# Kernel optimization log

Measured on AMD Instinct MI355X. Metric: run time of the kernel, lower is better.

The kernel has to match this reference:

```python
import jax, jax.numpy as jnp
import numpy as np

N = 40000
E = 640000
F_IN = 128
F_OUT = 128


def setup_inputs() -> dict:
    key = jax.random.key(0)
    ks = jax.random.split(key, 8)
    x = jax.random.normal(ks[0], (N, F_IN), dtype=jnp.float32)
    weight = jax.random.normal(ks[1], (F_IN, F_OUT), dtype=jnp.float32) * (1.0 / np.sqrt(F_OUT))
    node_w = jax.random.normal(ks[2], (F_IN, 1), dtype=jnp.float32)
    sem_w = jax.random.normal(ks[3], (F_IN,), dtype=jnp.float32) * (1.0 / np.sqrt(F_IN))
    bias = jax.random.normal(ks[4], (F_OUT,), dtype=jnp.float32) * 0.01
    adj_val = jax.random.uniform(ks[5], (E,), dtype=jnp.float32)
    src = jax.random.randint(ks[6], (E,), 0, N, dtype=jnp.int32)
    dst = jax.random.randint(ks[7], (E,), 0, N, dtype=jnp.int32)
    return {"x": x, "weight": weight, "node_w": node_w, "sem_w": sem_w,
            "bias": bias, "adj_val": adj_val, "src": src, "dst": dst}


def reference(x, weight, node_w, sem_w, bias, adj_val, src, dst):
    # node-level attention: per-node sigmoid scalar [N, 1]
    node_att = jax.nn.sigmoid(x @ node_w)
    # semantic-level attention: softmax over feature weight vector [F_in]
    sem_att = jax.nn.softmax(sem_w)
    # hierarchical weighting, then dense projection [N, F_out]
    support = (x * node_att * sem_att) @ weight
    # spmm(adj, support): COO aggregation, row=dst, col=src
    msg = support[src] * adj_val[:, None]  # [E, F_out]
    out = jax.ops.segment_sum(msg, dst, num_segments=N)
    return out + bias
```

## Files before the change

kernel.cpp:

```cpp
#include <hip/hip_runtime.h>
#include <hip/hip_bf16.h>

#define F 128
#define ROWS 32
#define CAP 64

typedef unsigned long long u64;

__global__ __launch_bounds__(256, 4) void support_kernel(
    const float* __restrict__ x, const float* __restrict__ weight,
    const float* __restrict__ node_w, const float* __restrict__ sem_w,
    float* __restrict__ support, int* __restrict__ cursor, int n_rows)
{
    __shared__ __align__(16) float xs[ROWS * F];
    __shared__ __align__(16) float sem[F];
    __shared__ float natt[ROWS];

    const int t = threadIdx.x;
    const int rbase = blockIdx.x * ROWS;

    if (cursor) {
        int gi = blockIdx.x * 256 + t;
        if (gi < n_rows) cursor[gi] = 0;
    }

    if (t < 64) {
        float v0 = sem_w[t], v1 = sem_w[t + 64];
        float m = fmaxf(v0, v1);
        #pragma unroll
        for (int off = 32; off; off >>= 1) m = fmaxf(m, __shfl_xor(m, off));
        float e0 = __expf(v0 - m), e1 = __expf(v1 - m);
        float ssum = e0 + e1;
        #pragma unroll
        for (int off = 32; off; off >>= 1) ssum += __shfl_xor(ssum, off);
        float inv = 1.0f / ssum;
        sem[t] = e0 * inv;
        sem[t + 64] = e1 * inv;
    }

    const int k4 = t & 31;
    float4 nw4 = ((const float4*)node_w)[k4];
    #pragma unroll
    for (int i = 0; i < 4; ++i) {
        int j = t + i * 256;
        int r = j >> 5;
        int gr = rbase + r;
        float4 v = make_float4(0.f, 0.f, 0.f, 0.f);
        if (gr < n_rows) v = ((const float4*)x)[(size_t)gr * 32 + k4];
        ((float4*)xs)[j] = v;
        float p = v.x * nw4.x + v.y * nw4.y + v.z * nw4.z + v.w * nw4.w;
        p += __shfl_xor(p, 1);  p += __shfl_xor(p, 2);  p += __shfl_xor(p, 4);
        p += __shfl_xor(p, 8);  p += __shfl_xor(p, 16);
        if ((t & 31) == 0) natt[r] = p;
    }
    __syncthreads();

    if (t < ROWS) {
        float z = natt[t];
        natt[t] = 1.0f / (1.0f + __expf(-z));
    }
    __syncthreads();

    #pragma unroll
    for (int i = 0; i < 4; ++i) {
        int j = t + i * 256;
        int r = j >> 5, kk = j & 31;
        float4 v = ((float4*)xs)[j];
        float4 s4 = ((float4*)sem)[kk];
        float a = natt[r];
        v.x *= a * s4.x; v.y *= a * s4.y; v.z *= a * s4.z; v.w *= a * s4.w;
        ((float4*)xs)[j] = v;
    }
    __syncthreads();

    const int cg = t & 31;
    const int rg = t >> 5;
    const float4* __restrict__ W4 = (const float4*)weight;
    float acc[4][4] = {};
    for (int k = 0; k < F; k += 4) {
        float4 w0 = W4[(k + 0) * 32 + cg];
        float4 w1 = W4[(k + 1) * 32 + cg];
        float4 w2 = W4[(k + 2) * 32 + cg];
        float4 w3 = W4[(k + 3) * 32 + cg];
        #pragma unroll
        for (int i = 0; i < 4; ++i) {
            float4 s = *(const float4*)&xs[(4 * rg + i) * F + k];
            acc[i][0] = fmaf(s.x, w0.x, acc[i][0]);
            acc[i][1] = fmaf(s.x, w0.y, acc[i][1]);
            acc[i][2] = fmaf(s.x, w0.z, acc[i][2]);
            acc[i][3] = fmaf(s.x, w0.w, acc[i][3]);
            acc[i][0] = fmaf(s.y, w1.x, acc[i][0]);
            acc[i][1] = fmaf(s.y, w1.y, acc[i][1]);
            acc[i][2] = fmaf(s.y, w1.z, acc[i][2]);
            acc[i][3] = fmaf(s.y, w1.w, acc[i][3]);
            acc[i][0] = fmaf(s.z, w2.x, acc[i][0]);
            acc[i][1] = fmaf(s.z, w2.y, acc[i][1]);
            acc[i][2] = fmaf(s.z, w2.z, acc[i][2]);
            acc[i][3] = fmaf(s.z, w2.w, acc[i][3]);
            acc[i][0] = fmaf(s.w, w3.x, acc[i][0]);
            acc[i][1] = fmaf(s.w, w3.y, acc[i][1]);
            acc[i][2] = fmaf(s.w, w3.z, acc[i][2]);
            acc[i][3] = fmaf(s.w, w3.w, acc[i][3]);
        }
    }

    #pragma unroll
    for (int i = 0; i < 4; ++i) {
        int r = rbase + 4 * rg + i;
        if (r < n_rows) {
            float4 o = make_float4(acc[i][0], acc[i][1], acc[i][2], acc[i][3]);
            ((float4*)support)[(size_t)r * 32 + cg] = o;
        }
    }
}

__global__ void append_kernel(const int* __restrict__ dst, const int* __restrict__ src,
                              const float* __restrict__ adj_val,
                              int* __restrict__ cursor, int2* __restrict__ payload, int e) {
    int i = blockIdx.x * blockDim.x + threadIdx.x;
    if (i < e) {
        int d = dst[i];
        int s = atomicAdd(&cursor[d], 1);
        if (s < CAP)
            payload[(size_t)d * CAP + s] = make_int2(src[i], __float_as_int(adj_val[i]));
    }
}

__global__ __launch_bounds__(256) void aggregate_kernel(
    const float* __restrict__ support, const int* __restrict__ cursor,
    const int2* __restrict__ payload, const float* __restrict__ bias,
    float* __restrict__ out, int Nn)
{
    const int gw = (int)((blockIdx.x * (unsigned)blockDim.x + threadIdx.x) >> 6);
    const int lane = threadIdx.x & 63;
    const int half = lane >> 5;
    const int l32  = lane & 31;
    if (gw >= Nn) return;
    int deg = cursor[gw];
    deg = deg > CAP ? CAP : deg;
    const int2* __restrict__ pay = payload + (size_t)gw * CAP;
    const float4* __restrict__ sup4 = (const float4*)support;

    float4 acc = make_float4(0.f, 0.f, 0.f, 0.f);
    int i = 0;
    for (; i + 8 <= deg; i += 8) {
        int2 p0 = pay[i + 0 + half];
        int2 p1 = pay[i + 2 + half];
        int2 p2 = pay[i + 4 + half];
        int2 p3 = pay[i + 6 + half];
        float4 v0 = sup4[(size_t)p0.x * 32 + l32];
        float4 v1 = sup4[(size_t)p1.x * 32 + l32];
        float4 v2 = sup4[(size_t)p2.x * 32 + l32];
        float4 v3 = sup4[(size_t)p3.x * 32 + l32];
        float a0 = __int_as_float(p0.y), a1 = __int_as_float(p1.y);
        float a2 = __int_as_float(p2.y), a3 = __int_as_float(p3.y);
        acc.x = fmaf(a0, v0.x, acc.x); acc.y = fmaf(a0, v0.y, acc.y);
        acc.z = fmaf(a0, v0.z, acc.z); acc.w = fmaf(a0, v0.w, acc.w);
        acc.x = fmaf(a1, v1.x, acc.x); acc.y = fmaf(a1, v1.y, acc.y);
        acc.z = fmaf(a1, v1.z, acc.z); acc.w = fmaf(a1, v1.w, acc.w);
        acc.x = fmaf(a2, v2.x, acc.x); acc.y = fmaf(a2, v2.y, acc.y);
        acc.z = fmaf(a2, v2.z, acc.z); acc.w = fmaf(a2, v2.w, acc.w);
        acc.x = fmaf(a3, v3.x, acc.x); acc.y = fmaf(a3, v3.y, acc.y);
        acc.z = fmaf(a3, v3.z, acc.z); acc.w = fmaf(a3, v3.w, acc.w);
    }
    for (; i + 2 <= deg; i += 2) {
        int2 p = pay[i + half];
        float4 v = sup4[(size_t)p.x * 32 + l32];
        float a = __int_as_float(p.y);
        acc.x = fmaf(a, v.x, acc.x); acc.y = fmaf(a, v.y, acc.y);
        acc.z = fmaf(a, v.z, acc.z); acc.w = fmaf(a, v.w, acc.w);
    }
    if (i < deg && half == 0) {
        int2 p = pay[i];
        float4 v = sup4[(size_t)p.x * 32 + l32];
        float a = __int_as_float(p.y);
        acc.x = fmaf(a, v.x, acc.x); acc.y = fmaf(a, v.y, acc.y);
        acc.z = fmaf(a, v.z, acc.z); acc.w = fmaf(a, v.w, acc.w);
    }

    acc.x += __shfl_xor(acc.x, 32);
    acc.y += __shfl_xor(acc.y, 32);
    acc.z += __shfl_xor(acc.z, 32);
    acc.w += __shfl_xor(acc.w, 32);

    if (half == 0) {
        float4 b = ((const float4*)bias)[l32];
        ((float4*)out)[(size_t)gw * 32 + l32] =
            make_float4(acc.x + b.x, acc.y + b.y, acc.z + b.z, acc.w + b.w);
    }
}

__global__ void init_out_kernel(float* __restrict__ out, const float* __restrict__ bias, int n) {
    int i = blockIdx.x * blockDim.x + threadIdx.x;
    if (i < n) out[i] = bias[i & (F - 1)];
}

__global__ void edge_atomic_kernel(const float* __restrict__ support,
                                   const int* __restrict__ src, const int* __restrict__ dst,
                                   const float* __restrict__ adj_val, float* __restrict__ out, int e) {
    long long g = (long long)blockIdx.x * blockDim.x + threadIdx.x;
    if (g >= (long long)e * 32) return;
    int ed = (int)(g >> 5), q = (int)(g & 31);
    float a = adj_val[ed];
    float4 v = ((const float4*)support)[(size_t)src[ed] * 32 + q];
    float* o = out + (size_t)dst[ed] * F + 4 * q;
    atomicAdd(o + 0, a * v.x);
    atomicAdd(o + 1, a * v.y);
    atomicAdd(o + 2, a * v.z);
    atomicAdd(o + 3, a * v.w);
}

extern "C" void kernel_launch(void* const* d_in, const int* in_sizes, int n_in,
                              void* d_out, int out_size, void* d_ws, size_t ws_size,
                              hipStream_t stream) {
    const float* x       = (const float*)d_in[0];
    const float* weight  = (const float*)d_in[1];
    const float* node_w  = (const float*)d_in[2];
    const float* sem_w   = (const float*)d_in[3];
    const float* bias    = (const float*)d_in[4];
    const float* adj_val = (const float*)d_in[5];
    const int*   src     = (const int*)d_in[6];
    const int*   dst     = (const int*)d_in[7];
    float* out = (float*)d_out;

    const int Nn = in_sizes[0] / F;
    const int Ee = in_sizes[5];

    char* ws = (char*)d_ws;
    size_t off = 0;
    auto alloc = [&](size_t bytes) {
        void* p = ws + off;
        off = (off + bytes + 255) & ~(size_t)255;
        return p;
    };
    float* support = (float*)alloc((size_t)Nn * F * sizeof(float));
    size_t need_atomic = off;
    int*  cursor  = (int*)alloc((size_t)Nn * sizeof(int));
    int2* payload = (int2*)alloc((size_t)Nn * CAP * sizeof(int2));
    size_t need_full = off;

    const bool full = (ws_size >= need_full);

    support_kernel<<<(Nn + ROWS - 1) / ROWS, 256, 0, stream>>>(
        x, weight, node_w, sem_w, support, full ? cursor : nullptr, Nn);

    if (full) {
        append_kernel<<<(Ee + 255) / 256, 256, 0, stream>>>(dst, src, adj_val,
                                                            cursor, payload, Ee);
        long long waves = (long long)Nn;
        int blocks = (int)((waves * 64 + 255) / 256);
        aggregate_kernel<<<blocks, 256, 0, stream>>>(
            support, cursor, payload, bias, out, Nn);
    } else if (ws_size >= need_atomic) {
        init_out_kernel<<<((size_t)Nn * F + 255) / 256, 256, 0, stream>>>(out, bias, Nn * F);
        long long tot = (long long)Ee * 32;
        edge_atomic_kernel<<<(unsigned)((tot + 255) / 256), 256, 0, stream>>>(
            support, src, dst, adj_val, out, Ee);
    }
}
```

Baseline: 106.7 us.

## Partition edge append by destination slice to localize atomics and payload writes

The append kernel becomes a fixed grid of 8 node slices by 104 edge chunks. Each block scans its chunk of dst with int2 loads and handles only edges whose destination falls in its slice. The aim is to keep the cursor atomics and payload scatter for concurrently running blocks within a smaller address range, which should improve cache and L2 locality. In exchange every dst entry is read 8 times, and the grid is fixed rather than scaled to E. The int2 load on dst+i assumes an even chunk start, which the even epb keeps aligned.

```diff
diff --git a/kernel.cpp b/kernel.cpp
--- a/kernel.cpp
+++ b/kernel.cpp
@@ -4,6 +4,8 @@
 #define F 128
 #define ROWS 32
 #define CAP 64
+#define NSLICE 8
+#define BPS 104
 
 typedef unsigned long long u64;
 
@@ -114,15 +116,44 @@
     }
 }
 
-__global__ void append_kernel(const int* __restrict__ dst, const int* __restrict__ src,
-                              const float* __restrict__ adj_val,
-                              int* __restrict__ cursor, int2* __restrict__ payload, int e) {
-    int i = blockIdx.x * blockDim.x + threadIdx.x;
-    if (i < e) {
-        int d = dst[i];
-        int s = atomicAdd(&cursor[d], 1);
-        if (s < CAP)
-            payload[(size_t)d * CAP + s] = make_int2(src[i], __float_as_int(adj_val[i]));
+__global__ __launch_bounds__(256) void append_kernel(
+    const int* __restrict__ dst, const int* __restrict__ src,
+    const float* __restrict__ adj_val,
+    int* __restrict__ cursor, int2* __restrict__ payload,
+    int e, int nodes_per_slice)
+{
+    const int slice = blockIdx.x % NSLICE;
+    const int chunk = blockIdx.x / NSLICE;
+    const int epb = ((e / (2 * BPS)) + 1) * 2;
+    const int c0 = chunk * epb;
+    const int c1 = min(c0 + epb, e);
+    const int lo = slice * nodes_per_slice;
+    const int hi = lo + nodes_per_slice;
+
+    for (int i = c0 + 2 * (int)threadIdx.x; i < c1; i += 2 * 256) {
+        if (i + 1 < c1) {
+            int2 d = *(const int2*)(dst + i);
+            if (d.x >= lo && d.x < hi) {
+                int s = atomicAdd(&cursor[d.x], 1);
+                if (s < CAP)
+                    payload[(size_t)d.x * CAP + s] =
+                        make_int2(src[i], __float_as_int(adj_val[i]));
+            }
+            if (d.y >= lo && d.y < hi) {
+                int s = atomicAdd(&cursor[d.y], 1);
+                if (s < CAP)
+                    payload[(size_t)d.y * CAP + s] =
+                        make_int2(src[i + 1], __float_as_int(adj_val[i + 1]));
+            }
+        } else {
+            int d = dst[i];
+            if (d >= lo && d < hi) {
+                int s = atomicAdd(&cursor[d], 1);
+                if (s < CAP)
+                    payload[(size_t)d * CAP + s] =
+                        make_int2(src[i], __float_as_int(adj_val[i]));
+            }
+        }
     }
 }
 
@@ -245,8 +276,9 @@
         x, weight, node_w, sem_w, support, full ? cursor : nullptr, Nn);
 
     if (full) {
-        append_kernel<<<(Ee + 255) / 256, 256, 0, stream>>>(dst, src, adj_val,
-                                                            cursor, payload, Ee);
+        const int nodes_per_slice = (Nn + NSLICE - 1) / NSLICE;
+        append_kernel<<<NSLICE * BPS, 256, 0, stream>>>(
+            dst, src, adj_val, cursor, payload, Ee, nodes_per_slice);
         long long waves = (long long)Nn;
         int blocks = (int)((waves * 64 + 255) / 256);
         aggregate_kernel<<<blocks, 256, 0, stream>>>(
```

Result: no change. 108.8 us (+1.9%).

## Partition edges into destination slices before building per-node payload buckets

Applied to the files above, without the earlier changes.

Replaces the single append kernel, which did scattered global atomics across all nodes, with two passes. A partition pass groups edges into 8 destination-range slices using LDS counters and one global atomic per slice per block, packing src, local dst and weight into a 64-bit record. A build pass then fills the per-node buckets slice by slice, meant to keep cursor atomics and payload writes localised for better cache behaviour. This adds an extra kernel launch, a large queue buffer sized 8×E, and an extra read and write of every edge.

```diff
diff --git a/kernel.cpp b/kernel.cpp
--- a/kernel.cpp
+++ b/kernel.cpp
@@ -4,13 +4,16 @@
 #define F 128
 #define ROWS 32
 #define CAP 64
+#define NSLICE 8
+#define BPB 128
 
 typedef unsigned long long u64;
 
 __global__ __launch_bounds__(256, 4) void support_kernel(
     const float* __restrict__ x, const float* __restrict__ weight,
     const float* __restrict__ node_w, const float* __restrict__ sem_w,
-    float* __restrict__ support, int* __restrict__ cursor, int n_rows)
+    float* __restrict__ support, int* __restrict__ cursor,
+    int* __restrict__ qcur, int n_rows)
 {
     __shared__ __align__(16) float xs[ROWS * F];
     __shared__ __align__(16) float sem[F];
@@ -22,6 +25,7 @@
     if (cursor) {
         int gi = blockIdx.x * 256 + t;
         if (gi < n_rows) cursor[gi] = 0;
+        if (blockIdx.x == 0 && t < NSLICE) qcur[t] = 0;
     }
 
     if (t < 64) {
@@ -114,15 +118,73 @@
     }
 }
 
-__global__ void append_kernel(const int* __restrict__ dst, const int* __restrict__ src,
-                              const float* __restrict__ adj_val,
-                              int* __restrict__ cursor, int2* __restrict__ payload, int e) {
-    int i = blockIdx.x * blockDim.x + threadIdx.x;
-    if (i < e) {
-        int d = dst[i];
+__global__ __launch_bounds__(256) void partition_kernel(
+    const int* __restrict__ dst, const int* __restrict__ src,
+    const float* __restrict__ adj_val,
+    int* __restrict__ qcur, u64* __restrict__ queue,
+    int e, int nps, int qcap)
+{
+    __shared__ int lc[NSLICE];
+    __shared__ int lbase[NSLICE];
+    const int t = threadIdx.x;
+    const int b0 = blockIdx.x * 512;
+
+    if (t < NSLICE) lc[t] = 0;
+    __syncthreads();
+
+    int s0 = -1, s1 = -1, sl0 = 0, sl1 = 0;
+    int2 dd = make_int2(0, 0), ss = make_int2(0, 0);
+    float2 aa = make_float2(0.f, 0.f);
+    int i0 = b0 + 2 * t;
+    if (i0 + 1 < e) {
+        dd = ((const int2*)dst)[b0 / 2 + t];
+        ss = ((const int2*)src)[b0 / 2 + t];
+        aa = ((const float2*)adj_val)[b0 / 2 + t];
+        s0 = dd.x / nps;
+        s1 = dd.y / nps;
+        sl0 = atomicAdd(&lc[s0], 1);
+        sl1 = atomicAdd(&lc[s1], 1);
+    } else if (i0 < e) {
+        dd.x = dst[i0]; ss.x = src[i0]; aa.x = adj_val[i0];
+        s0 = dd.x / nps;
+        sl0 = atomicAdd(&lc[s0], 1);
+    }
+    __syncthreads();
+    if (t < NSLICE) lbase[t] = atomicAdd(&qcur[t], lc[t]);
+    __syncthreads();
+
+    if (s0 >= 0) {
+        u64 r = (u64)(unsigned)(ss.x & 0xFFFF)
+              | ((u64)(unsigned)(dd.x - s0 * nps) << 16)
+              | ((u64)(unsigned)__float_as_int(aa.x) << 32);
+        queue[(size_t)s0 * qcap + lbase[s0] + sl0] = r;
+    }
+    if (s1 >= 0) {
+        u64 r = (u64)(unsigned)(ss.y & 0xFFFF)
+              | ((u64)(unsigned)(dd.y - s1 * nps) << 16)
+              | ((u64)(unsigned)__float_as_int(aa.y) << 32);
+        queue[(size_t)s1 * qcap + lbase[s1] + sl1] = r;
+    }
+}
+
+__global__ __launch_bounds__(256) void build_kernel(
+    const int* __restrict__ qcur, const u64* __restrict__ queue,
+    int* __restrict__ cursor, int2* __restrict__ payload,
+    int nps, int qcap)
+{
+    const int slice = blockIdx.x % NSLICE;
+    const int k     = blockIdx.x / NSLICE;
+    const int qn = qcur[slice];
+    const int lo = slice * nps;
+    const u64* __restrict__ q = queue + (size_t)slice * qcap;
+
+    for (int i = k * 256 + (int)threadIdx.x; i < qn; i += BPB * 256) {
+        u64 r = q[i];
+        int sc = (int)(r & 0xFFFF);
+        int d  = lo + (int)((r >> 16) & 0xFFFF);
+        int ab = (int)(unsigned)(r >> 32);
         int s = atomicAdd(&cursor[d], 1);
-        if (s < CAP)
-            payload[(size_t)d * CAP + s] = make_int2(src[i], __float_as_int(adj_val[i]));
+        if (s < CAP) payload[(size_t)d * CAP + s] = make_int2(sc, ab);
     }
 }
 
@@ -236,17 +298,24 @@
     float* support = (float*)alloc((size_t)Nn * F * sizeof(float));
     size_t need_atomic = off;
     int*  cursor  = (int*)alloc((size_t)Nn * sizeof(int));
+    int*  qcur    = (int*)alloc(NSLICE * sizeof(int));
     int2* payload = (int2*)alloc((size_t)Nn * CAP * sizeof(int2));
+    const int qcap = Ee;
+    u64*  queue   = (u64*)alloc((size_t)NSLICE * qcap * sizeof(u64));
     size_t need_full = off;
 
-    const bool full = (ws_size >= need_full);
+    const bool full = (ws_size >= need_full) && (Nn < 65536);
 
     support_kernel<<<(Nn + ROWS - 1) / ROWS, 256, 0, stream>>>(
-        x, weight, node_w, sem_w, support, full ? cursor : nullptr, Nn);
+        x, weight, node_w, sem_w, support,
+        full ? cursor : nullptr, qcur, Nn);
 
     if (full) {
-        append_kernel<<<(Ee + 255) / 256, 256, 0, stream>>>(dst, src, adj_val,
-                                                            cursor, payload, Ee);
+        const int nps = (Nn + NSLICE - 1) / NSLICE;
+        partition_kernel<<<(Ee + 511) / 512, 256, 0, stream>>>(
+            dst, src, adj_val, qcur, queue, Ee, nps, qcap);
+        build_kernel<<<NSLICE * BPB, 256, 0, stream>>>(
+            qcur, queue, cursor, payload, nps, qcap);
         long long waves = (long long)Nn;
         int blocks = (int)((waves * 64 + 255) / 256);
         aggregate_kernel<<<blocks, 256, 0, stream>>>(
```

Result: slower. 121.0 us (+13.4%).
